# Optimization experiments

Hardware: AMD Instinct MI355X
Metric: run time of the kernel (lower is better)

Reference implementation:

```python
import jax, jax.numpy as jnp
import numpy as np

BEV_H, BEV_W, BEV_Z = 100, 100, 4
PC_RANGE = (-51.2, -51.2, -5.0, 51.2, 51.2, 3.0)
EPS = 1e-5
N_CAM, C_DIM, H_IMG, W_IMG, BATCH = 6, 256, 32, 88, 1


def _make_lidar2img(n_cam, h_img, w_img):
    # Realistic rig: n_cam cameras at equal yaw spacing, ~70 deg HFOV,
    # intrinsics expressed in feature-map pixel units.
    fx = w_img / (2.0 * np.tan(np.deg2rad(35.0)))
    fy = fx
    cx, cy = w_img / 2.0, h_img / 2.0
    K = np.array([[fx, 0, cx, 0], [0, fy, cy, 0], [0, 0, 1, 0], [0, 0, 0, 1]], np.float32)
    mats = []
    for i in range(n_cam):
        th = 2.0 * np.pi * i / n_cam
        c, s = np.cos(th), np.sin(th)
        # camera: z forward (world yaw th), x right, y down; camera at ego origin
        R = np.array([[-s, c, 0.0], [0.0, 0.0, -1.0], [c, s, 0.0]], np.float32)
        T = np.eye(4, dtype=np.float32)
        T[:3, :3] = R
        mats.append(K @ T)
    return np.stack(mats)[None]  # (1, n_cam, 4, 4)


def get_reference_points(H, W, Z, bs):
    ref_y, ref_x = jnp.meshgrid(
        jnp.linspace(0.5, H - 0.5, H, dtype=jnp.float32),
        jnp.linspace(0.5, W - 0.5, W, dtype=jnp.float32), indexing='ij')
    ref_y = (ref_y.reshape(-1) / H)[None, :, None]          # (1, HW, 1)
    ref_x = (ref_x.reshape(-1) / W)[None, :, None]
    ref_x = jnp.broadcast_to(ref_x, (1, H * W, Z))
    ref_y = jnp.broadcast_to(ref_y, (1, H * W, Z))
    ref_z = jnp.broadcast_to(jnp.linspace(0.5, Z - 0.5, Z, dtype=jnp.float32)[None, None, :], (1, H * W, Z))
    ref_3d = jnp.stack((ref_x, ref_y, ref_z), -1)           # (1, HW, Z, 3)
    return jnp.broadcast_to(ref_3d, (bs, H * W, Z, 3))


def bilinear_sample(img, gx, gy):
    # img: (BN, C, H, W); gx, gy in [-1, 1]: (BN, P)
    # F.grid_sample bilinear, padding_mode='zeros', align_corners=False
    BN, C, H, W = img.shape
    x = (gx + 1.0) * W * 0.5 - 0.5
    y = (gy + 1.0) * H * 0.5 - 0.5
    x0 = jnp.floor(x)
    y0 = jnp.floor(y)
    wx1 = x - x0
    wy1 = y - y0
    flat = img.reshape(BN, C, H * W)

    def corner(xi, yi, w):
        valid = (xi >= 0) & (xi < W) & (yi >= 0) & (yi < H)
        xc = jnp.clip(xi, 0, W - 1).astype(jnp.int32)
        yc = jnp.clip(yi, 0, H - 1).astype(jnp.int32)
        idx = yc * W + xc                                   # (BN, P)
        idx = jnp.broadcast_to(idx[:, None, :], (BN, C, idx.shape[-1]))
        vals = jnp.take_along_axis(flat, idx, axis=2)       # (BN, C, P)
        return vals * (w * valid.astype(img.dtype))[:, None, :]

    out = corner(x0, y0, (1 - wx1) * (1 - wy1))
    out = out + corner(x0 + 1, y0, wx1 * (1 - wy1))
    out = out + corner(x0, y0 + 1, (1 - wx1) * wy1)
    out = out + corner(x0 + 1, y0 + 1, wx1 * wy1)
    return out


def setup_inputs() -> dict:
    key = jax.random.key(0)
    k0, k1, k2, k3 = jax.random.split(key, 4)
    Nq = BEV_H * BEV_W
    query = jax.random.normal(k0, (BATCH, Nq, C_DIM), jnp.float32)
    img_feats = jax.random.normal(k1, (BATCH, N_CAM, C_DIM, H_IMG, W_IMG), jnp.float32)
    lidar2img = jnp.asarray(_make_lidar2img(N_CAM, H_IMG, W_IMG))
    W_out = jax.random.normal(k2, (C_DIM, C_DIM), jnp.float32) * 0.02
    b_out = jax.random.normal(k3, (C_DIM,), jnp.float32) * 0.02
    return {'query': query, 'img_feats': img_feats, 'lidar2img': lidar2img,
            'W_out': W_out, 'b_out': b_out}


def reference(query, img_feats, lidar2img, W_out, b_out):
    B, Nq, C = query.shape
    N_cam, _, H_img, W_img = img_feats.shape[1], img_feats.shape[2], img_feats.shape[3], img_feats.shape[4]
    Z = BEV_Z
    pc = PC_RANGE

    ref = get_reference_points(BEV_H, BEV_W, Z, B)          # (B, Nq, Z, 3) normalized
    ref = jnp.stack([
        ref[..., 0] * (pc[3] - pc[0]) + pc[0],
        ref[..., 1] * (pc[4] - pc[1]) + pc[1],
        ref[..., 2] * (pc[5] - pc[2]) + pc[2],
    ], axis=-1)
    pts = jnp.concatenate([ref, jnp.ones_like(ref[..., :1])], -1)  # (B, Nq, Z, 4)
    pts = pts.reshape(B, Nq * Z, 4)
    # project: (B, N_cam, P, 4)
    cam = jnp.einsum('bnij,bpj->bnpi', lidar2img, pts)
    z = cam[..., 2:3]
    mask = z > EPS
    xy = cam[..., 0:2] / jnp.maximum(z, EPS)
    gx = (xy[..., 0] / W_img - 0.5) * 2.0                    # (B, N_cam, P)
    gy = (xy[..., 1] / H_img - 0.5) * 2.0
    mask = (mask[..., 0] & (gx > -1.0) & (gx < 1.0) & (gy > -1.0) & (gy < 1.0))

    img_flat = img_feats.reshape(B * N_cam, C, H_img, W_img)
    sampled = bilinear_sample(img_flat, gx.reshape(B * N_cam, -1), gy.reshape(B * N_cam, -1))
    sampled = sampled.reshape(B, N_cam, C, Nq, Z)
    sampled = jnp.nan_to_num(sampled * mask.reshape(B, N_cam, 1, Nq, Z).astype(sampled.dtype))

    w = jnp.mean(sampled, axis=1)                            # (B, C, Nq, Z) mean over cams
    w = jnp.mean(w, axis=3)                                  # (B, C, Nq) mean over Z
    out = jnp.transpose(w, (0, 2, 1))                        # (B, Nq, C)
    return out @ W_out.T + b_out + query
```

## Files before the change

### kernel.cpp

```cpp
#include <hip/hip_runtime.h>
#include <hip/hip_bf16.h>
#include <math.h>

#define BEV_H 100
#define BEV_W 100
#define BEV_Z 4
#define N_CAM 6
#define C_DIM 256
#define H_IMG 32
#define W_IMG 88
#define NQ (BEV_H * BEV_W)
#define HW_IMG (H_IMG * W_IMG)

typedef float f32x4 __attribute__((ext_vector_type(4)));
typedef short short8 __attribute__((ext_vector_type(8)));

__device__ __forceinline__ unsigned short f2b(float f) {
    __hip_bfloat16 h = __float2bfloat16(f);
    return *reinterpret_cast<unsigned short*>(&h);
}
__device__ __forceinline__ float b2f(unsigned short u) {
    return __uint_as_float((unsigned int)u << 16);
}

__global__ __launch_bounds__(256) void prep_kernel(const float* __restrict__ img,
                                                   unsigned short* __restrict__ imgT) {
    __shared__ unsigned short tile[32][68];
    int cam = blockIdx.z;
    int t = threadIdx.x;
    int hw0 = blockIdx.x * 32;
    int c0  = blockIdx.y * 64;
    const float* src = img + (size_t)cam * C_DIM * HW_IMG;
    #pragma unroll
    for (int i = 0; i < 2; ++i) {
        int e = i * 256 + t;
        int c  = e >> 3;
        int hq = e & 7;
        float4 v = *(const float4*)(src + (size_t)(c0 + c) * HW_IMG + hw0 + hq * 4);
        tile[hq * 4 + 0][c] = f2b(v.x);
        tile[hq * 4 + 1][c] = f2b(v.y);
        tile[hq * 4 + 2][c] = f2b(v.z);
        tile[hq * 4 + 3][c] = f2b(v.w);
    }
    __syncthreads();
    unsigned short* dst = imgT + (size_t)cam * HW_IMG * C_DIM;
    #pragma unroll
    for (int i = 0; i < 2; ++i) {
        int e = i * 256 + t;
        int hw = e >> 4;
        int cq = e & 15;
        ushort4 o;
        o.x = tile[hw][cq * 4 + 0];
        o.y = tile[hw][cq * 4 + 1];
        o.z = tile[hw][cq * 4 + 2];
        o.w = tile[hw][cq * 4 + 3];
        *(ushort4*)(dst + (size_t)(hw0 + hw) * C_DIM + c0 + cq * 4) = o;
    }
}

__global__ __launch_bounds__(256) void sample_kernel(const unsigned short* __restrict__ imgT,
                                                     const float* __restrict__ l2i,
                                                     unsigned short* __restrict__ wbuf) {
    __shared__ int   ent_off[4][24][4];
    __shared__ float ent_w[4][24][4];
    __shared__ int   counts[4];
    int t = threadIdx.x;

    if (t < 128) {
        int ql   = t >> 5;
        int slot = t & 31;
        int q = blockIdx.x * 4 + ql;
        int ix = q % BEV_W;
        int iy = q / BEV_W;
        float x = ((ix + 0.5f) / (float)BEV_W) * 102.4f - 51.2f;
        float y = ((iy + 0.5f) / (float)BEV_H) * 102.4f - 51.2f;

        bool valid = false;
        int   o0 = 0, o1 = 0, o2 = 0, o3 = 0;
        float w0 = 0.f, w1 = 0.f, w2 = 0.f, w3 = 0.f;
        if (slot < 24) {
            int cam = slot >> 2;
            int zi  = slot & 3;
            const float* L = l2i + cam * 16;
            float zl = (zi + 0.5f) * 8.0f - 5.0f;
            float cx = fmaf(L[0], x, fmaf(L[1], y, fmaf(L[2],  zl, L[3])));
            float cy = fmaf(L[4], x, fmaf(L[5], y, fmaf(L[6],  zl, L[7])));
            float cz = fmaf(L[8], x, fmaf(L[9], y, fmaf(L[10], zl, L[11])));
            float denom = fmaxf(cz, 1e-5f);
            float inv = __builtin_amdgcn_rcpf(denom);
            float u = cx * inv;
            float v = cy * inv;
            if ((cz > 1e-5f) && (u > 0.f) && (u < (float)W_IMG)
                             && (v > 0.f) && (v < (float)H_IMG)) {
                valid = true;
                float xs = u - 0.5f;
                float ys = v - 0.5f;
                float x0f = floorf(xs), y0f = floorf(ys);
                float wx1 = xs - x0f,   wy1 = ys - y0f;
                float wx0 = 1.0f - wx1, wy0 = 1.0f - wy1;
                int x0 = (int)x0f, y0 = (int)y0f;
                int x1 = x0 + 1,   y1 = y0 + 1;
                float mxl = (x0 >= 0)     ? 1.f : 0.f;
                float mxh = (x1 < W_IMG)  ? 1.f : 0.f;
                float myl = (y0 >= 0)     ? 1.f : 0.f;
                float myh = (y1 < H_IMG)  ? 1.f : 0.f;
                int x0c = max(x0, 0), x1c = min(x1, W_IMG - 1);
                int y0c = max(y0, 0), y1c = min(y1, H_IMG - 1);
                int cbase = cam * HW_IMG;
                o0 = (cbase + y0c * W_IMG + x0c) << 9;  w0 = (wx0 * mxl) * (wy0 * myl);
                o1 = (cbase + y0c * W_IMG + x1c) << 9;  w1 = (wx1 * mxh) * (wy0 * myl);
                o2 = (cbase + y1c * W_IMG + x0c) << 9;  w2 = (wx0 * mxl) * (wy1 * myh);
                o3 = (cbase + y1c * W_IMG + x1c) << 9;  w3 = (wx1 * mxh) * (wy1 * myh);
            }
        }
        unsigned long long bal = __ballot(valid);
        unsigned int half = (t & 32) ? (unsigned int)(bal >> 32) : (unsigned int)bal;
        int lane32 = t & 31;
        int pre = __popc(half & ((1u << lane32) - 1u));
        if (valid) {
            ent_off[ql][pre][0] = o0; ent_off[ql][pre][1] = o1;
            ent_off[ql][pre][2] = o2; ent_off[ql][pre][3] = o3;
            ent_w[ql][pre][0] = w0; ent_w[ql][pre][1] = w1;
            ent_w[ql][pre][2] = w2; ent_w[ql][pre][3] = w3;
        }
        if (lane32 == 0) counts[ql] = __popc(half);
    }
    __syncthreads();

    int wav  = t >> 6;
    int lane = t & 63;
    int q = blockIdx.x * 4 + wav;
    int cnt = counts[wav];
    const char* base = (const char*)imgT + lane * 8;

    float a0 = 0.f, a1 = 0.f, a2 = 0.f, a3 = 0.f;
    for (int i = 0; i < cnt; ++i) {
        int4   offs = *(const int4*)(&ent_off[wav][i][0]);
        float4 wv   = *(const float4*)(&ent_w[wav][i][0]);
        ushort4 f0 = *(const ushort4*)(base + offs.x);
        ushort4 f1 = *(const ushort4*)(base + offs.y);
        ushort4 f2 = *(const ushort4*)(base + offs.z);
        ushort4 f3 = *(const ushort4*)(base + offs.w);
        a0 += b2f(f0.x) * wv.x; a1 += b2f(f0.y) * wv.x;
        a2 += b2f(f0.z) * wv.x; a3 += b2f(f0.w) * wv.x;
        a0 += b2f(f1.x) * wv.y; a1 += b2f(f1.y) * wv.y;
        a2 += b2f(f1.z) * wv.y; a3 += b2f(f1.w) * wv.y;
        a0 += b2f(f2.x) * wv.z; a1 += b2f(f2.y) * wv.z;
        a2 += b2f(f2.z) * wv.z; a3 += b2f(f2.w) * wv.z;
        a0 += b2f(f3.x) * wv.w; a1 += b2f(f3.y) * wv.w;
        a2 += b2f(f3.z) * wv.w; a3 += b2f(f3.w) * wv.w;
    }
    const float s = 1.0f / 24.0f;
    ushort4 o;
    o.x = f2b(a0 * s); o.y = f2b(a1 * s); o.z = f2b(a2 * s); o.w = f2b(a3 * s);
    *(ushort4*)(wbuf + (size_t)q * C_DIM + lane * 4) = o;
}

#define BM 64
#define BN 64
#define BKK 128
__global__ __launch_bounds__(256) void gemm_kernel(const unsigned short* __restrict__ A,
                                                   const float* __restrict__ Wout,
                                                   const float* __restrict__ bout,
                                                   const float* __restrict__ query,
                                                   float* __restrict__ out) {
    __shared__ unsigned short Al[BM * BKK];
    __shared__ unsigned short Bl[BN * BKK];
    int rb = blockIdx.x * BM;
    int cb = blockIdx.y * BN;
    int t = threadIdx.x;
    int lane = t & 63;
    int wid = t >> 6;
    int wr = wid >> 1, wc = wid & 1;
    int fr = lane & 15;
    int kq = lane >> 4;

    f32x4 acc[2][2] = {};

    for (int kt = 0; kt < C_DIM; kt += BKK) {
        #pragma unroll
        for (int i = 0; i < 4; ++i) {
            int idx = i * 256 + t;
            int row = idx >> 4;
            int ch  = idx & 15;
            int4 av = make_int4(0, 0, 0, 0);
            int grow = rb + row;
            if (grow < NQ) av = *(const int4*)(A + (size_t)grow * C_DIM + kt + ch * 8);
            int off = (row * 256 + ch * 16) ^ ((row & 7) << 4);
            *(int4*)((char*)Al + off) = av;
        }
        #pragma unroll
        for (int i = 0; i < 4; ++i) {
            int idx = i * 256 + t;
            int row = idx >> 4;
            int ch  = idx & 15;
            const float* bs = Wout + (size_t)(cb + row) * C_DIM + kt + ch * 8;
            float4 b0 = *(const float4*)(bs);
            float4 b1 = *(const float4*)(bs + 4);
            ushort4 plo, phi;
            plo.x = f2b(b0.x); plo.y = f2b(b0.y); plo.z = f2b(b0.z); plo.w = f2b(b0.w);
            phi.x = f2b(b1.x); phi.y = f2b(b1.y); phi.z = f2b(b1.z); phi.w = f2b(b1.w);
            int off = (row * 256 + ch * 16) ^ ((row & 7) << 4);
            *(ushort4*)((char*)Bl + off)     = plo;
            *(ushort4*)((char*)Bl + off + 8) = phi;
        }
        __syncthreads();

        #pragma unroll
        for (int ks = 0; ks < 4; ++ks) {
            int kbyte = ks * 64 + kq * 16;
            int ra0 = wr * 32 + fr, ra1 = ra0 + 16;
            int rb0 = wc * 32 + fr, rb1 = rb0 + 16;
            short8 af0 = *(const short8*)((const char*)Al + ((ra0 * 256 + kbyte) ^ ((ra0 & 7) << 4)));
            short8 af1 = *(const short8*)((const char*)Al + ((ra1 * 256 + kbyte) ^ ((ra1 & 7) << 4)));
            short8 bf0 = *(const short8*)((const char*)Bl + ((rb0 * 256 + kbyte) ^ ((rb0 & 7) << 4)));
            short8 bf1 = *(const short8*)((const char*)Bl + ((rb1 * 256 + kbyte) ^ ((rb1 & 7) << 4)));
            acc[0][0] = __builtin_amdgcn_mfma_f32_16x16x32_bf16(af0, bf0, acc[0][0], 0, 0, 0);
            acc[0][1] = __builtin_amdgcn_mfma_f32_16x16x32_bf16(af0, bf1, acc[0][1], 0, 0, 0);
            acc[1][0] = __builtin_amdgcn_mfma_f32_16x16x32_bf16(af1, bf0, acc[1][0], 0, 0, 0);
            acc[1][1] = __builtin_amdgcn_mfma_f32_16x16x32_bf16(af1, bf1, acc[1][1], 0, 0, 0);
        }
        __syncthreads();
    }

    int crow = (lane >> 4) * 4;
    int ccol = lane & 15;
    #pragma unroll
    for (int fi = 0; fi < 2; ++fi) {
        #pragma unroll
        for (int fj = 0; fj < 2; ++fj) {
            int n = cb + wc * 32 + fj * 16 + ccol;
            float bn = bout[n];
            #pragma unroll
            for (int r = 0; r < 4; ++r) {
                int m = rb + wr * 32 + fi * 16 + crow + r;
                if (m < NQ) {
                    size_t off = (size_t)m * C_DIM + n;
                    out[off] = acc[fi][fj][r] + bn + query[off];
                }
            }
        }
    }
}

extern "C" void kernel_launch(void* const* d_in, const int* in_sizes, int n_in,
                              void* d_out, int out_size, void* d_ws, size_t ws_size,
                              hipStream_t stream) {
    const float* query = (const float*)d_in[0];
    const float* img   = (const float*)d_in[1];
    const float* l2i   = (const float*)d_in[2];
    const float* Wout  = (const float*)d_in[3];
    const float* bout  = (const float*)d_in[4];
    float* out = (float*)d_out;

    unsigned short* imgT = (unsigned short*)d_ws;
    unsigned short* wbuf = (unsigned short*)((char*)d_ws + 8650752);

    dim3 gP(HW_IMG / 32, C_DIM / 64, N_CAM);
    prep_kernel<<<gP, 256, 0, stream>>>(img, imgT);

    sample_kernel<<<NQ / 4, 256, 0, stream>>>(imgT, l2i, wbuf);

    dim3 gG((NQ + BM - 1) / BM, C_DIM / BN);
    gemm_kernel<<<gG, 256, 0, stream>>>(wbuf, Wout, bout, query, out);
}
```

Measured before the change: 29.84 us.

## Pre-convert Wout to bf16 in prep kernel and widen sample gathers to 16B

The prep kernel gains an extra grid slice that converts the fp32 output projection weights to bf16 once, so each GEMM block loads bf16 B tiles directly instead of reloading and converting fp32 weights. The sampling kernel now handles 8 queries per block with 32 lanes per query, each gathering 16-byte chunks (8 channels), which halves the number of gather instructions and uses all threads in the projection phase. The trade-off is an extra workspace buffer, some idle blocks in the enlarged prep grid, and more registers per thread in the sampler.

```diff
diff --git a/kernel.cpp b/kernel.cpp
--- a/kernel.cpp
+++ b/kernel.cpp
@@ -19,15 +19,30 @@
     __hip_bfloat16 h = __float2bfloat16(f);
     return *reinterpret_cast<unsigned short*>(&h);
 }
-__device__ __forceinline__ float b2f(unsigned short u) {
-    return __uint_as_float((unsigned int)u << 16);
+__device__ __forceinline__ float b2f_lo(unsigned int u) {
+    return __uint_as_float(u << 16);
+}
+__device__ __forceinline__ float b2f_hi(unsigned int u) {
+    return __uint_as_float(u & 0xffff0000u);
 }
 
 __global__ __launch_bounds__(256) void prep_kernel(const float* __restrict__ img,
-                                                   unsigned short* __restrict__ imgT) {
-    __shared__ unsigned short tile[32][68];
+                                                   const float* __restrict__ Wout,
+                                                   unsigned short* __restrict__ imgT,
+                                                   unsigned short* __restrict__ Woutb) {
     int cam = blockIdx.z;
     int t = threadIdx.x;
+    if (cam == N_CAM) {
+        if (blockIdx.y == 0 && blockIdx.x < 64) {
+            int base = (blockIdx.x * 256 + t) * 4;
+            float4 v = *(const float4*)(Wout + base);
+            ushort4 o;
+            o.x = f2b(v.x); o.y = f2b(v.y); o.z = f2b(v.z); o.w = f2b(v.w);
+            *(ushort4*)(Woutb + base) = o;
+        }
+        return;
+    }
+    __shared__ unsigned short tile[32][68];
     int hw0 = blockIdx.x * 32;
     int c0  = blockIdx.y * 64;
     const float* src = img + (size_t)cam * C_DIM * HW_IMG;
@@ -61,15 +76,15 @@
 __global__ __launch_bounds__(256) void sample_kernel(const unsigned short* __restrict__ imgT,
                                                      const float* __restrict__ l2i,
                                                      unsigned short* __restrict__ wbuf) {
-    __shared__ int   ent_off[4][24][4];
-    __shared__ float ent_w[4][24][4];
-    __shared__ int   counts[4];
+    __shared__ int   ent_off[8][24][4];
+    __shared__ float ent_w[8][24][4];
+    __shared__ int   counts[8];
     int t = threadIdx.x;
 
-    if (t < 128) {
+    {
         int ql   = t >> 5;
         int slot = t & 31;
-        int q = blockIdx.x * 4 + ql;
+        int q = blockIdx.x * 8 + ql;
         int ix = q % BEV_W;
         int iy = q / BEV_W;
         float x = ((ix + 0.5f) / (float)BEV_W) * 102.4f - 51.2f;
@@ -127,40 +142,52 @@
     }
     __syncthreads();
 
-    int wav  = t >> 6;
-    int lane = t & 63;
-    int q = blockIdx.x * 4 + wav;
-    int cnt = counts[wav];
-    const char* base = (const char*)imgT + lane * 8;
+    int qi = t >> 5;
+    int lane32 = t & 31;
+    int q = blockIdx.x * 8 + qi;
+    int cnt = counts[qi];
+    const char* base = (const char*)imgT + lane32 * 16;
 
     float a0 = 0.f, a1 = 0.f, a2 = 0.f, a3 = 0.f;
+    float a4 = 0.f, a5 = 0.f, a6 = 0.f, a7 = 0.f;
     for (int i = 0; i < cnt; ++i) {
-        int4   offs = *(const int4*)(&ent_off[wav][i][0]);
-        float4 wv   = *(const float4*)(&ent_w[wav][i][0]);
-        ushort4 f0 = *(const ushort4*)(base + offs.x);
-        ushort4 f1 = *(const ushort4*)(base + offs.y);
-        ushort4 f2 = *(const ushort4*)(base + offs.z);
-        ushort4 f3 = *(const ushort4*)(base + offs.w);
-        a0 += b2f(f0.x) * wv.x; a1 += b2f(f0.y) * wv.x;
-        a2 += b2f(f0.z) * wv.x; a3 += b2f(f0.w) * wv.x;
-        a0 += b2f(f1.x) * wv.y; a1 += b2f(f1.y) * wv.y;
-        a2 += b2f(f1.z) * wv.y; a3 += b2f(f1.w) * wv.y;
-        a0 += b2f(f2.x) * wv.z; a1 += b2f(f2.y) * wv.z;
-        a2 += b2f(f2.z) * wv.z; a3 += b2f(f2.w) * wv.z;
-        a0 += b2f(f3.x) * wv.w; a1 += b2f(f3.y) * wv.w;
-        a2 += b2f(f3.z) * wv.w; a3 += b2f(f3.w) * wv.w;
+        int4   offs = *(const int4*)(&ent_off[qi][i][0]);
+        float4 wv   = *(const float4*)(&ent_w[qi][i][0]);
+        int4 f0 = *(const int4*)(base + offs.x);
+        int4 f1 = *(const int4*)(base + offs.y);
+        int4 f2 = *(const int4*)(base + offs.z);
+        int4 f3 = *(const int4*)(base + offs.w);
+        a0 += b2f_lo(f0.x) * wv.x; a1 += b2f_hi(f0.x) * wv.x;
+        a2 += b2f_lo(f0.y) * wv.x; a3 += b2f_hi(f0.y) * wv.x;
+        a4 += b2f_lo(f0.z) * wv.x; a5 += b2f_hi(f0.z) * wv.x;
+        a6 += b2f_lo(f0.w) * wv.x; a7 += b2f_hi(f0.w) * wv.x;
+        a0 += b2f_lo(f1.x) * wv.y; a1 += b2f_hi(f1.x) * wv.y;
+        a2 += b2f_lo(f1.y) * wv.y; a3 += b2f_hi(f1.y) * wv.y;
+        a4 += b2f_lo(f1.z) * wv.y; a5 += b2f_hi(f1.z) * wv.y;
+        a6 += b2f_lo(f1.w) * wv.y; a7 += b2f_hi(f1.w) * wv.y;
+        a0 += b2f_lo(f2.x) * wv.z; a1 += b2f_hi(f2.x) * wv.z;
+        a2 += b2f_lo(f2.y) * wv.z; a3 += b2f_hi(f2.y) * wv.z;
+        a4 += b2f_lo(f2.z) * wv.z; a5 += b2f_hi(f2.z) * wv.z;
+        a6 += b2f_lo(f2.w) * wv.z; a7 += b2f_hi(f2.w) * wv.z;
+        a0 += b2f_lo(f3.x) * wv.w; a1 += b2f_hi(f3.x) * wv.w;
+        a2 += b2f_lo(f3.y) * wv.w; a3 += b2f_hi(f3.y) * wv.w;
+        a4 += b2f_lo(f3.z) * wv.w; a5 += b2f_hi(f3.z) * wv.w;
+        a6 += b2f_lo(f3.w) * wv.w; a7 += b2f_hi(f3.w) * wv.w;
     }
     const float s = 1.0f / 24.0f;
-    ushort4 o;
-    o.x = f2b(a0 * s); o.y = f2b(a1 * s); o.z = f2b(a2 * s); o.w = f2b(a3 * s);
-    *(ushort4*)(wbuf + (size_t)q * C_DIM + lane * 4) = o;
+    int4 o;
+    o.x = (int)f2b(a0 * s) | ((int)f2b(a1 * s) << 16);
+    o.y = (int)f2b(a2 * s) | ((int)f2b(a3 * s) << 16);
+    o.z = (int)f2b(a4 * s) | ((int)f2b(a5 * s) << 16);
+    o.w = (int)f2b(a6 * s) | ((int)f2b(a7 * s) << 16);
+    *(int4*)(wbuf + (size_t)q * C_DIM + lane32 * 8) = o;
 }
 
 #define BM 64
 #define BN 64
 #define BKK 128
 __global__ __launch_bounds__(256) void gemm_kernel(const unsigned short* __restrict__ A,
-                                                   const float* __restrict__ Wout,
+                                                   const unsigned short* __restrict__ B,
                                                    const float* __restrict__ bout,
                                                    const float* __restrict__ query,
                                                    float* __restrict__ out) {
@@ -186,23 +213,10 @@
             int4 av = make_int4(0, 0, 0, 0);
             int grow = rb + row;
             if (grow < NQ) av = *(const int4*)(A + (size_t)grow * C_DIM + kt + ch * 8);
+            int4 bv = *(const int4*)(B + (size_t)(cb + row) * C_DIM + kt + ch * 8);
             int off = (row * 256 + ch * 16) ^ ((row & 7) << 4);
             *(int4*)((char*)Al + off) = av;
-        }
-        #pragma unroll
-        for (int i = 0; i < 4; ++i) {
-            int idx = i * 256 + t;
-            int row = idx >> 4;
-            int ch  = idx & 15;
-            const float* bs = Wout + (size_t)(cb + row) * C_DIM + kt + ch * 8;
-            float4 b0 = *(const float4*)(bs);
-            float4 b1 = *(const float4*)(bs + 4);
-            ushort4 plo, phi;
-            plo.x = f2b(b0.x); plo.y = f2b(b0.y); plo.z = f2b(b0.z); plo.w = f2b(b0.w);
-            phi.x = f2b(b1.x); phi.y = f2b(b1.y); phi.z = f2b(b1.z); phi.w = f2b(b1.w);
-            int off = (row * 256 + ch * 16) ^ ((row & 7) << 4);
-            *(ushort4*)((char*)Bl + off)     = plo;
-            *(ushort4*)((char*)Bl + off + 8) = phi;
+            *(int4*)((char*)Bl + off) = bv;
         }
         __syncthreads();
 
@@ -253,14 +267,15 @@
     const float* bout  = (const float*)d_in[4];
     float* out = (float*)d_out;
 
-    unsigned short* imgT = (unsigned short*)d_ws;
-    unsigned short* wbuf = (unsigned short*)((char*)d_ws + 8650752);
-
-    dim3 gP(HW_IMG / 32, C_DIM / 64, N_CAM);
-    prep_kernel<<<gP, 256, 0, stream>>>(img, imgT);
-
-    sample_kernel<<<NQ / 4, 256, 0, stream>>>(imgT, l2i, wbuf);
+    unsigned short* imgT  = (unsigned short*)d_ws;
+    unsigned short* wbuf  = (unsigned short*)((char*)d_ws + 8650752);
+    unsigned short* Woutb = (unsigned short*)((char*)d_ws + 13770752);
+
+    dim3 gP(HW_IMG / 32, C_DIM / 64, N_CAM + 1);
+    prep_kernel<<<gP, 256, 0, stream>>>(img, Wout, imgT, Woutb);
+
+    sample_kernel<<<NQ / 8, 256, 0, stream>>>(imgT, l2i, wbuf);
 
     dim3 gG((NQ + BM - 1) / BM, C_DIM / BN);
-    gemm_kernel<<<gG, 256, 0, stream>>>(wbuf, Wout, bout, query, out);
-}
+    gemm_kernel<<<gG, 256, 0, stream>>>(wbuf, Woutb, bout, query, out);
+}
```

Measured after the change: 28.67 us. -3.9%, faster.
